# Optimization experiments

Hardware: AMD Instinct MI355X
Metric: run time of the kernel (lower is better)

Reference implementation:

```python
import jax, jax.numpy as jnp
import numpy as np

B, T, C, F, E, K = 4, 2048, 1024, 4096, 8, 2
CAP_FACTOR = 1.0
AUX_COEF = 0.01
CAPACITY = max(1, int(CAP_FACTOR * (B * T) * max(1, K) / E + 0.9999))


def setup_inputs() -> dict:
    key = jax.random.key(0)
    ks = jax.random.split(key, 4)
    s = 0.02
    return {
        "x": jax.random.normal(ks[0], (B, T, C), jnp.float32),
        "w_gate": jax.random.normal(ks[1], (C, E), jnp.float32) * s,
        "b_gate": jnp.zeros((E,), jnp.float32),
        "W1": jax.random.normal(ks[2], (E, C, F), jnp.float32) * s,
        "b1": jnp.zeros((E, F), jnp.float32),
        "W2": jax.random.normal(ks[3], (E, F, C), jnp.float32) * s,
        "b2": jnp.zeros((E, C), jnp.float32),
    }


def reference(x, w_gate, b_gate, W1, b1, W2, b2):
    Bb, Tt, Cc = x.shape
    N = Bb * Tt
    S = N * K  # dispatch slots, token-major with k inner (matches the python double loop order)
    x_flat = x.reshape(N, Cc)

    # Top-K gating
    logits = x_flat @ w_gate + b_gate                       # [N, E]
    probs = jax.nn.softmax(logits, axis=-1)
    topk_w, topk_idx = jax.lax.top_k(probs, K)              # [N, K]
    topk_w = topk_w / (topk_w.sum(-1, keepdims=True) + 1e-9)

    e_flat = topk_idx.reshape(S)                            # expert id per slot
    w_flat = topk_w.reshape(S)
    tok = jnp.arange(S) // K                                # source token per slot

    # First-come-first-served capacity: position of each slot within its expert
    onehot = jax.nn.one_hot(e_flat, E, dtype=jnp.int32)     # [S, E]
    pos_in_e = (jnp.cumsum(onehot, axis=0) - onehot)        # exclusive count per expert
    pos_in_e = (pos_in_e * onehot).sum(-1)                  # [S]
    keep = pos_in_e < CAPACITY
    keepf = keep.astype(x.dtype)
    p_safe = jnp.where(keep, pos_in_e, CAPACITY - 1)        # dropped slots scatter zeros

    # Dispatch -> [E, capacity, C]
    disp = jnp.zeros((E, CAPACITY, Cc), x.dtype).at[e_flat, p_safe].add(
        x_flat[tok] * keepf[:, None]
    )

    # Per-expert FFN (grouped GEMM)
    h = jax.nn.gelu(jnp.einsum("epc,ecf->epf", disp, W1) + b1[:, None, :])
    y = jnp.einsum("epf,efc->epc", h, W2) + b2[:, None, :]  # [E, capacity, C]

    # Combine: gather each kept slot's expert output, weight, scatter-add back to tokens
    y_slot = y[e_flat, p_safe] * (w_flat * keepf)[:, None]  # [S, C]
    out = jnp.zeros((N, Cc), x.dtype).at[tok].add(y_slot).reshape(Bb, Tt, Cc)

    # Load-balancing aux loss (expert_load is detached in the original)
    expert_load = jnp.sum(onehot.astype(jnp.float32) * keepf[:, None], axis=0)  # [E]
    expert_load = jax.lax.stop_gradient(expert_load)
    frac_expected = probs.mean(axis=0)
    frac_expected = frac_expected / (frac_expected.sum() + 1e-9)
    frac_actual = expert_load / (expert_load.sum() + 1e-9)
    aux_loss = AUX_COEF * jnp.mean((frac_expected - frac_actual) ** 2)

    return out, aux_loss
```

## Files before the change

### kernel.cpp

```cpp
#include <hip/hip_runtime.h>
#include <hip/hip_bf16.h>
#include <math.h>


#define DEV __device__ __forceinline__

typedef __attribute__((ext_vector_type(4))) float f32x4;
typedef __attribute__((ext_vector_type(8))) short bf16x8;

constexpr int B_ = 4, T_ = 2048, C_ = 1024, F_ = 4096, E_ = 8, TOPK_ = 2;
constexpr int N_ = B_ * T_;
constexpr int S_ = N_ * TOPK_;
constexpr int CAP_ = 2048;

#define GLOAD16(G, L)                                              \
  __builtin_amdgcn_global_load_lds(                                \
      (const __attribute__((address_space(1))) void*)(G),          \
      (__attribute__((address_space(3))) void*)(L), 16, 0, 0)

DEV float gelu_tanh(float x) {
  float x3 = x * x * x;
  float u = 0.7978845608028654f * (x + 0.044715f * x3);
  return 0.5f * x * (1.0f + tanhf(u));
}


__global__ __launch_bounds__(256) void cvt_x_kernel(
    const float* __restrict__ in, __hip_bfloat16* __restrict__ out, int n4) {
  int i = blockIdx.x * 256 + threadIdx.x;
  if (i >= n4) return;
  float4 v = ((const float4*)in)[i];
  __hip_bfloat16 o[4] = {__float2bfloat16(v.x), __float2bfloat16(v.y),
                         __float2bfloat16(v.z), __float2bfloat16(v.w)};
  *(uint2*)(out + (size_t)i * 4) = *(uint2*)o;
}

__global__ __launch_bounds__(256) void transpose_cvt_kernel(
    const float* __restrict__ in, __hip_bfloat16* __restrict__ out, int R, int S) {
  __shared__ float tile[32][33];
  int e = blockIdx.z;
  int s0 = blockIdx.x * 32;
  int r0 = blockIdx.y * 32;
  int tx = threadIdx.x & 31;
  int ty = threadIdx.x >> 5;
  const float* ip = in + (size_t)e * R * S;
  __hip_bfloat16* op = out + (size_t)e * R * S;
#pragma unroll
  for (int i = 0; i < 32; i += 8)
    tile[ty + i][tx] = ip[(size_t)(r0 + ty + i) * S + s0 + tx];
  __syncthreads();
#pragma unroll
  for (int i = 0; i < 32; i += 8)
    op[(size_t)(s0 + ty + i) * R + r0 + tx] = __float2bfloat16(tile[tx][ty + i]);
}


__global__ __launch_bounds__(256) void gate_kernel(
    const float* __restrict__ x, const float* __restrict__ wg,
    const float* __restrict__ bg, int* __restrict__ slot_e,
    float* __restrict__ slot_w, float* __restrict__ probs_sum) {
  int lane = threadIdx.x & 63;
  int wv = threadIdx.x >> 6;
  int wid = blockIdx.x * 4 + wv;
  float psum[E_];
#pragma unroll
  for (int e = 0; e < E_; ++e) psum[e] = 0.f;

  for (int ti = 0; ti < 8; ++ti) {
    int t = wid * 8 + ti;
    const float* xr = x + (size_t)t * C_;
    float acc[E_];
#pragma unroll
    for (int e = 0; e < E_; ++e) acc[e] = 0.f;
    for (int c = lane; c < C_; c += 64) {
      float xv = xr[c];
      const float* wr = wg + (size_t)c * E_;
#pragma unroll
      for (int e = 0; e < E_; ++e) acc[e] += xv * wr[e];
    }
#pragma unroll
    for (int e = 0; e < E_; ++e) {
#pragma unroll
      for (int off = 32; off >= 1; off >>= 1)
        acc[e] += __shfl_xor(acc[e], off, 64);
    }
    if (lane == 0) {
      float lg[E_], p[E_];
      float mx = -1e30f;
#pragma unroll
      for (int e = 0; e < E_; ++e) { lg[e] = acc[e] + bg[e]; mx = fmaxf(mx, lg[e]); }
      float s = 0.f;
#pragma unroll
      for (int e = 0; e < E_; ++e) { p[e] = expf(lg[e] - mx); s += p[e]; }
      float inv = 1.f / s;
#pragma unroll
      for (int e = 0; e < E_; ++e) { p[e] *= inv; psum[e] += p[e]; }
      int i1 = 0; float p1 = p[0];
#pragma unroll
      for (int e = 1; e < E_; ++e) if (p[e] > p1) { p1 = p[e]; i1 = e; }
      int i2 = -1; float p2 = -1.f;
#pragma unroll
      for (int e = 0; e < E_; ++e) if (e != i1 && p[e] > p2) { p2 = p[e]; i2 = e; }
      float wden = 1.f / (p1 + p2 + 1e-9f);
      slot_e[2 * t] = i1;     slot_w[2 * t] = p1 * wden;
      slot_e[2 * t + 1] = i2; slot_w[2 * t + 1] = p2 * wden;
    }
  }
  if (lane == 0) {
#pragma unroll
    for (int e = 0; e < E_; ++e) atomicAdd(&probs_sum[e], psum[e]);
  }
}


__global__ __launch_bounds__(256) void scan_kernel(
    const int* __restrict__ slot_e, const float* __restrict__ slot_w,
    int* __restrict__ idx_list, float* __restrict__ w_list,
    const float* __restrict__ probs_sum, float* __restrict__ aux_out) {
  __shared__ int sc[256][E_];
  int tid = threadIdx.x;
  int s0 = tid * 64;
  int cnt[E_];
#pragma unroll
  for (int e = 0; e < E_; ++e) cnt[e] = 0;
  for (int j = 0; j < 64; ++j) cnt[slot_e[s0 + j]]++;
#pragma unroll
  for (int e = 0; e < E_; ++e) sc[tid][e] = cnt[e];
  __syncthreads();
  for (int off = 1; off < 256; off <<= 1) {
    int v[E_];
    bool act = (tid >= off);
    if (act) {
#pragma unroll
      for (int e = 0; e < E_; ++e) v[e] = sc[tid - off][e];
    }
    __syncthreads();
    if (act) {
#pragma unroll
      for (int e = 0; e < E_; ++e) sc[tid][e] += v[e];
    }
    __syncthreads();
  }
  int base[E_];
#pragma unroll
  for (int e = 0; e < E_; ++e) base[e] = tid ? sc[tid - 1][e] : 0;
  for (int j = 0; j < 64; ++j) {
    int s = s0 + j;
    int e = slot_e[s];
    int p = base[e]++;
    if (p < CAP_) {
      idx_list[e * CAP_ + p] = s >> 1;
      w_list[e * CAP_ + p] = slot_w[s];
    }
  }
  if (tid == 0) {
    float fe[E_], fa[E_], fs = 0.f, ls = 0.f;
#pragma unroll
    for (int e = 0; e < E_; ++e) {
      fe[e] = probs_sum[e] / (float)N_;
      fs += fe[e];
      int tot = sc[255][e];
      fa[e] = (float)(tot < CAP_ ? tot : CAP_);
      ls += fa[e];
    }
    float i1 = 1.f / (fs + 1e-9f), i2 = 1.f / (ls + 1e-9f);
    float a = 0.f;
#pragma unroll
    for (int e = 0; e < E_; ++e) {
      float d = fe[e] * i1 - fa[e] * i2;
      a += d * d;
    }
    aux_out[0] = 0.01f * a / (float)E_;
  }
}


template <int EPI, bool GATHER>
__global__ __launch_bounds__(512, 2) void gemm256(
    const __hip_bfloat16* __restrict__ Aall,
    const __hip_bfloat16* __restrict__ Ball,
    const int* __restrict__ idxl,
    const float* __restrict__ wl,
    const float* __restrict__ bias,
    void* __restrict__ Cout,
    const __hip_bfloat16* __restrict__ zrow,
    int Ndim, int Kdim, int ncol) {
  __shared__ __align__(16) __hip_bfloat16 lds[2][2][256 * 64];

  const int nwg = gridDim.x;
  const int wg = ((int)blockIdx.x & 7) * (nwg >> 3) + ((int)blockIdx.x >> 3);
  const int e = wg / (ncol * 8);
  const int rem = wg - e * (ncol * 8);
  const int x = rem >> 3, y = rem & 7;
  const int row0 = y * 256, col0 = x * 256;

  const int tid = threadIdx.x;
  const int lane = tid & 63;
  const int w = tid >> 6;
  const int wm = w >> 2, wn = w & 3;

  const int cb = ((lane & 7) * 16) ^ ((lane >> 5) << 5);
  const int rch = w * 8 + (lane >> 3);
  const __hip_bfloat16* srcA[4];
  const __hip_bfloat16* srcB[4];
  const __hip_bfloat16* Be = Ball + (size_t)e * Ndim * Kdim;
#pragma unroll
  for (int c = 0; c < 4; ++c) {
    int r = c * 64 + rch;
    if (GATHER) {
      int tok = idxl[e * CAP_ + row0 + r];
      srcA[c] = ((tok >= 0) ? Aall + (size_t)tok * Kdim : zrow) + (cb >> 1);
    } else {
      srcA[c] = Aall + ((size_t)e * CAP_ + row0 + r) * Kdim + (cb >> 1);
    }
    srcB[c] = Be + (size_t)(col0 + r) * Kdim + (cb >> 1);
  }
  const int dstoff = w * 512;

  const int sxor = (lane & 4) << 3;
  const int rA = wm * 128 + (lane & 15);
  const int rB = wn * 64 + (lane & 15);
  const int kb = (lane >> 4) * 16;

  f32x4 acc[8][4];
#pragma unroll
  for (int i = 0; i < 8; ++i)
#pragma unroll
    for (int j = 0; j < 4; ++j) acc[i][j] = (f32x4){0.f, 0.f, 0.f, 0.f};

  const int NT = Kdim >> 6;

#define STAGE_TILE(PAR, T)                                        \
  {                                                               \
    const int k0_ = (T) * 64;                                     \
    _Pragma("unroll") for (int c = 0; c < 4; ++c) {               \
      GLOAD16(srcA[c] + k0_, &lds[PAR][0][c * 4096 + dstoff]);    \
      GLOAD16(srcB[c] + k0_, &lds[PAR][1][c * 4096 + dstoff]);    \
    }                                                             \
  }

  STAGE_TILE(0, 0);
  asm volatile("s_waitcnt vmcnt(0)" ::: "memory");
  __builtin_amdgcn_sched_barrier(0);
  __builtin_amdgcn_s_barrier();
  __builtin_amdgcn_sched_barrier(0);

  for (int t = 0; t < NT; ++t) {
    const int par = t & 1;
    const char* baseA = (const char*)&lds[par][0][0];
    const char* baseB = (const char*)&lds[par][1][0];
    bf16x8 bfr[4][2];
#pragma unroll
    for (int q = 0; q < 4; ++q) {
      if (q == 0) {
#pragma unroll
        for (int n = 0; n < 4; ++n)
#pragma unroll
          for (int ks = 0; ks < 2; ++ks)
            bfr[n][ks] = *(const bf16x8*)(
                baseB + ((((rB + n * 16) * 128) + ks * 64 + kb) ^ sxor));
      }
      bf16x8 af[2][2];
#pragma unroll
      for (int i = 0; i < 2; ++i)
#pragma unroll
        for (int ks = 0; ks < 2; ++ks)
          af[i][ks] = *(const bf16x8*)(
              baseA + ((((rA + (q * 2 + i) * 16) * 128) + ks * 64 + kb) ^ sxor));
      if (q == 0 && t + 1 < NT) STAGE_TILE(par ^ 1, t + 1);
      __builtin_amdgcn_s_barrier();
      __builtin_amdgcn_s_setprio(1);
#pragma unroll
      for (int ks = 0; ks < 2; ++ks)
#pragma unroll
        for (int i = 0; i < 2; ++i)
#pragma unroll
          for (int n = 0; n < 4; ++n)
            acc[q * 2 + i][n] = __builtin_amdgcn_mfma_f32_16x16x32_bf16(
                af[i][ks], bfr[n][ks], acc[q * 2 + i][n], 0, 0, 0);
      __builtin_amdgcn_s_setprio(0);
      __builtin_amdgcn_s_barrier();
    }
    asm volatile("s_waitcnt vmcnt(0)" ::: "memory");
    __builtin_amdgcn_sched_barrier(0);
    __builtin_amdgcn_s_barrier();
    __builtin_amdgcn_sched_barrier(0);
  }
#undef STAGE_TILE

  const float* brow = bias + (size_t)e * Ndim;
  const int orow0 = row0 + wm * 128 + (lane >> 4) * 4;
  const int ocol0 = col0 + wn * 64 + (lane & 15);
  if (EPI == 0) {
    __hip_bfloat16* H = (__hip_bfloat16*)Cout + (size_t)e * CAP_ * Ndim;
#pragma unroll
    for (int mi = 0; mi < 8; ++mi)
#pragma unroll
      for (int n = 0; n < 4; ++n) {
        int cc = ocol0 + n * 16;
        float bv = brow[cc];
#pragma unroll
        for (int j = 0; j < 4; ++j) {
          int rr = orow0 + mi * 16 + j;
          H[(size_t)rr * Ndim + cc] = __float2bfloat16(gelu_tanh(acc[mi][n][j] + bv));
        }
      }
  } else {
    float* outp = (float*)Cout;
#pragma unroll
    for (int mi = 0; mi < 8; ++mi)
#pragma unroll
      for (int j = 0; j < 4; ++j) {
        int rr = orow0 + mi * 16 + j;
        int tk = idxl[e * CAP_ + rr];
        if (tk < 0) continue;
        float ww = wl[e * CAP_ + rr];
#pragma unroll
        for (int n = 0; n < 4; ++n) {
          int cc = ocol0 + n * 16;
          unsafeAtomicAdd(&outp[(size_t)tk * C_ + cc], ww * (acc[mi][n][j] + brow[cc]));
        }
      }
  }
}


extern "C" void kernel_launch(void* const* d_in, const int* in_sizes, int n_in,
                              void* d_out, int out_size, void* d_ws,
                              size_t ws_size, hipStream_t stream) {
  (void)in_sizes; (void)n_in; (void)out_size; (void)ws_size;
  const float* x = (const float*)d_in[0];
  const float* w_gate = (const float*)d_in[1];
  const float* b_gate = (const float*)d_in[2];
  const float* W1 = (const float*)d_in[3];
  const float* b1 = (const float*)d_in[4];
  const float* W2 = (const float*)d_in[5];
  const float* b2 = (const float*)d_in[6];
  float* out = (float*)d_out;

  char* p = (char*)d_ws;
  __hip_bfloat16* xb = (__hip_bfloat16*)p;
  __hip_bfloat16* W1t = (__hip_bfloat16*)(p + ((size_t)16 << 20));
  __hip_bfloat16* W2t = (__hip_bfloat16*)p;
  __hip_bfloat16* Hb = (__hip_bfloat16*)(p + ((size_t)80 << 20));
  char* meta = p + ((size_t)208 << 20);
  int* slot_e = (int*)meta;
  float* slot_w = (float*)(meta + (64 << 10));
  int* idx_list = (int*)(meta + (128 << 10));
  float* w_list = (float*)(meta + (192 << 10));
  float* probs_sum = (float*)(meta + (256 << 10));
  __hip_bfloat16* zrow = (__hip_bfloat16*)(meta + (260 << 10));

  hipMemsetAsync(idx_list, 0xFF, E_ * CAP_ * sizeof(int), stream);
  hipMemsetAsync(probs_sum, 0, E_ * sizeof(float), stream);
  hipMemsetAsync(zrow, 0, 16 << 10, stream);
  hipMemsetAsync(out, 0, (size_t)N_ * C_ * sizeof(float), stream);

  cvt_x_kernel<<<(N_ * C_ / 4 + 255) / 256, 256, 0, stream>>>(x, xb, N_ * C_ / 4);
  transpose_cvt_kernel<<<dim3(F_ / 32, C_ / 32, E_), 256, 0, stream>>>(W1, W1t, C_, F_);
  gate_kernel<<<N_ / 32, 256, 0, stream>>>(x, w_gate, b_gate, slot_e, slot_w, probs_sum);
  scan_kernel<<<1, 256, 0, stream>>>(slot_e, slot_w, idx_list, w_list, probs_sum,
                                     out + (size_t)N_ * C_);
  gemm256<0, true><<<16 * 8 * E_, 512, 0, stream>>>(
      xb, W1t, idx_list, nullptr, b1, Hb, zrow, F_, C_, 16);
  transpose_cvt_kernel<<<dim3(C_ / 32, F_ / 32, E_), 256, 0, stream>>>(W2, W2t, F_, C_);
  gemm256<1, false><<<4 * 8 * E_, 512, 0, stream>>>(
      Hb, W2t, idx_list, w_list, b2, out, zrow, C_, F_, 4);
}
```

Measured before the change: 977.9 us.

## Split prefetch waits per A-half and widen LDS XOR swizzle in grouped GEMM

Reorders the global-to-LDS loads so the A chunks needed by the first two compute phases arrive first. The single end-of-tile full drain is replaced by partial vmcnt waits, so the next tile's later A chunks can still be in flight while the earlier phases compute. The LDS swizzle changes from a 2-way to a full 8-way XOR across the row's 16-byte chunks, aiming to cut bank conflicts on the fragment reads. In exchange it relies on precise in-order vmcnt accounting, which is fragile if load order or count ever changes.

Measured after the change: 955.4 us. 2.3% less time.

```diff
diff --git a/kernel.cpp b/kernel.cpp
--- a/kernel.cpp
+++ b/kernel.cpp
@@ -199,8 +199,8 @@
   const int w = tid >> 6;
   const int wm = w >> 2, wn = w & 3;
 
-  const int cb = ((lane & 7) * 16) ^ ((lane >> 5) << 5);
   const int rch = w * 8 + (lane >> 3);
+  const int cbe = ((lane & 7) ^ (lane >> 3)) << 3;
   const __hip_bfloat16* srcA[4];
   const __hip_bfloat16* srcB[4];
   const __hip_bfloat16* Be = Ball + (size_t)e * Ndim * Kdim;
@@ -209,15 +209,15 @@
     int r = c * 64 + rch;
     if (GATHER) {
       int tok = idxl[e * CAP_ + row0 + r];
-      srcA[c] = ((tok >= 0) ? Aall + (size_t)tok * Kdim : zrow) + (cb >> 1);
+      srcA[c] = ((tok >= 0) ? Aall + (size_t)tok * Kdim : zrow) + cbe;
     } else {
-      srcA[c] = Aall + ((size_t)e * CAP_ + row0 + r) * Kdim + (cb >> 1);
-    }
-    srcB[c] = Be + (size_t)(col0 + r) * Kdim + (cb >> 1);
+      srcA[c] = Aall + ((size_t)e * CAP_ + row0 + r) * Kdim + cbe;
+    }
+    srcB[c] = Be + (size_t)(col0 + r) * Kdim + cbe;
   }
   const int dstoff = w * 512;
 
-  const int sxor = (lane & 4) << 3;
+  const int sxor = (lane & 7) << 4;
   const int rA = wm * 128 + (lane & 15);
   const int rB = wn * 64 + (lane & 15);
   const int kb = (lane >> 4) * 16;
@@ -230,63 +230,79 @@
 
   const int NT = Kdim >> 6;
 
-#define STAGE_TILE(PAR, T)                                        \
+#define STAGE(PAR, T)                                             \
   {                                                               \
     const int k0_ = (T) * 64;                                     \
-    _Pragma("unroll") for (int c = 0; c < 4; ++c) {               \
-      GLOAD16(srcA[c] + k0_, &lds[PAR][0][c * 4096 + dstoff]);    \
-      GLOAD16(srcB[c] + k0_, &lds[PAR][1][c * 4096 + dstoff]);    \
-    }                                                             \
-  }
-
-  STAGE_TILE(0, 0);
+    GLOAD16(srcB[0] + k0_, &lds[PAR][1][0 * 4096 + dstoff]);      \
+    GLOAD16(srcB[1] + k0_, &lds[PAR][1][1 * 4096 + dstoff]);      \
+    GLOAD16(srcB[2] + k0_, &lds[PAR][1][2 * 4096 + dstoff]);      \
+    GLOAD16(srcB[3] + k0_, &lds[PAR][1][3 * 4096 + dstoff]);      \
+    GLOAD16(srcA[0] + k0_, &lds[PAR][0][0 * 4096 + dstoff]);      \
+    GLOAD16(srcA[2] + k0_, &lds[PAR][0][2 * 4096 + dstoff]);      \
+    GLOAD16(srcA[1] + k0_, &lds[PAR][0][1 * 4096 + dstoff]);      \
+    GLOAD16(srcA[3] + k0_, &lds[PAR][0][3 * 4096 + dstoff]);      \
+  }
+
+#define PHASE_READ(Q)                                                       \
+  _Pragma("unroll") for (int i = 0; i < 2; ++i)                             \
+      _Pragma("unroll") for (int ks = 0; ks < 2; ++ks)                      \
+          af[i][ks] = *(const bf16x8*)(baseA +                              \
+              ((((rA + ((Q)*2 + i) * 16) * 128) + ks * 64 + kb) ^ sxor));
+
+#define PHASE_MFMA(Q)                                                       \
+  __builtin_amdgcn_s_barrier();                                             \
+  __builtin_amdgcn_s_setprio(1);                                            \
+  _Pragma("unroll") for (int ks = 0; ks < 2; ++ks)                          \
+      _Pragma("unroll") for (int i = 0; i < 2; ++i)                         \
+          _Pragma("unroll") for (int n = 0; n < 4; ++n)                     \
+              acc[(Q)*2 + i][n] = __builtin_amdgcn_mfma_f32_16x16x32_bf16(  \
+                  af[i][ks], bfr[n][ks], acc[(Q)*2 + i][n], 0, 0, 0);       \
+  __builtin_amdgcn_s_setprio(0);
+
+  STAGE(0, 0);
   asm volatile("s_waitcnt vmcnt(0)" ::: "memory");
   __builtin_amdgcn_sched_barrier(0);
   __builtin_amdgcn_s_barrier();
-  __builtin_amdgcn_sched_barrier(0);
 
   for (int t = 0; t < NT; ++t) {
     const int par = t & 1;
+    const bool pre = (t + 1 < NT);
     const char* baseA = (const char*)&lds[par][0][0];
     const char* baseB = (const char*)&lds[par][1][0];
     bf16x8 bfr[4][2];
-#pragma unroll
-    for (int q = 0; q < 4; ++q) {
-      if (q == 0) {
-#pragma unroll
-        for (int n = 0; n < 4; ++n)
-#pragma unroll
-          for (int ks = 0; ks < 2; ++ks)
-            bfr[n][ks] = *(const bf16x8*)(
-                baseB + ((((rB + n * 16) * 128) + ks * 64 + kb) ^ sxor));
-      }
-      bf16x8 af[2][2];
-#pragma unroll
-      for (int i = 0; i < 2; ++i)
-#pragma unroll
-        for (int ks = 0; ks < 2; ++ks)
-          af[i][ks] = *(const bf16x8*)(
-              baseA + ((((rA + (q * 2 + i) * 16) * 128) + ks * 64 + kb) ^ sxor));
-      if (q == 0 && t + 1 < NT) STAGE_TILE(par ^ 1, t + 1);
-      __builtin_amdgcn_s_barrier();
-      __builtin_amdgcn_s_setprio(1);
+    bf16x8 af[2][2];
+
+    if (pre) STAGE(par ^ 1, t + 1);
+#pragma unroll
+    for (int n = 0; n < 4; ++n)
 #pragma unroll
       for (int ks = 0; ks < 2; ++ks)
-#pragma unroll
-        for (int i = 0; i < 2; ++i)
-#pragma unroll
-          for (int n = 0; n < 4; ++n)
-            acc[q * 2 + i][n] = __builtin_amdgcn_mfma_f32_16x16x32_bf16(
-                af[i][ks], bfr[n][ks], acc[q * 2 + i][n], 0, 0, 0);
-      __builtin_amdgcn_s_setprio(0);
-      __builtin_amdgcn_s_barrier();
-    }
-    asm volatile("s_waitcnt vmcnt(0)" ::: "memory");
+        bfr[n][ks] = *(const bf16x8*)(baseB +
+            ((((rB + n * 16) * 128) + ks * 64 + kb) ^ sxor));
+    PHASE_READ(0);
+    PHASE_MFMA(0);
+    __builtin_amdgcn_s_barrier();
+
+    PHASE_READ(1);
+    PHASE_MFMA(1);
+    if (pre) asm volatile("s_waitcnt vmcnt(8)" ::: "memory");
+    else     asm volatile("s_waitcnt vmcnt(0)" ::: "memory");
     __builtin_amdgcn_sched_barrier(0);
     __builtin_amdgcn_s_barrier();
+
+    PHASE_READ(2);
+    PHASE_MFMA(2);
+    __builtin_amdgcn_s_barrier();
+
+    PHASE_READ(3);
+    PHASE_MFMA(3);
+    asm volatile("s_waitcnt vmcnt(2)" ::: "memory");
     __builtin_amdgcn_sched_barrier(0);
-  }
-#undef STAGE_TILE
+    __builtin_amdgcn_s_barrier();
+  }
+#undef STAGE
+#undef PHASE_READ
+#undef PHASE_MFMA
 
   const float* brow = bias + (size_t)e * Ndim;
   const int orow0 = row0 + wm * 128 + (lane >> 4) * 4;
```
